# Performance work log

Hardware: AMD Instinct MI355X
Metric: run time of the kernel (lower is better)

## Reference

```python
import jax, jax.numpy as jnp
import numpy as np
import math

N_CELLS = 65536
HIDDEN = 128
IN_DIM = 64
MAX_DEG = 6
BOND_P = 0.5


def _build_graph():
    """2D lattice bond percolation -> padded adjacency [n, MAX_DEG] + signs + mask."""
    rng = np.random.default_rng(0)
    side = int(math.ceil(math.sqrt(N_CELLS)))
    adj = [[] for _ in range(N_CELLS)]
    for i in range(N_CELLS):
        col = i % side
        r = i + 1
        if col + 1 < side and r < N_CELLS and rng.random() < BOND_P:
            adj[i].append(r); adj[r].append(i)
        d = i + side
        if d < N_CELLS and rng.random() < BOND_P:
            adj[i].append(d); adj[d].append(i)
    for i in range(N_CELLS):  # ring fix for isolated nodes
        if not adj[i]:
            r = (i + 1) % N_CELLS
            adj[i].append(r); adj[r].append(i)
    sign_map = {}
    for i in range(N_CELLS):
        for j in adj[i]:
            key = (min(i, j), max(i, j))
            if key not in sign_map:
                sign_map[key] = 1.0 if rng.random() > 0.5 else -1.0
    nbr = np.zeros((N_CELLS, MAX_DEG), np.int32)
    sgn = np.ones((N_CELLS, MAX_DEG), np.float32)
    msk = np.zeros((N_CELLS, MAX_DEG), bool)
    for i in range(N_CELLS):
        for k, j in enumerate(adj[i][:MAX_DEG]):
            nbr[i, k] = j
            msk[i, k] = True
            sgn[i, k] = sign_map[(min(i, j), max(i, j))]
    return nbr, sgn, msk


def setup_inputs() -> dict:
    key = jax.random.key(0)
    ks = jax.random.split(key, 8)
    nbr, sgn, msk = _build_graph()
    n = N_CELLS
    cell_amp = jax.random.uniform(ks[0], (n, HIDDEN)) * 0.5 + 0.5
    cell_phase = jax.random.normal(ks[1], (n, HIDDEN)) * 0.5 \
        + (2.0 * jnp.pi * jnp.arange(n, dtype=jnp.float32) / n)[:, None]
    phase_vel = jax.random.normal(ks[2], (n, HIDDEN)) * 0.05
    return {
        'x': jax.random.normal(ks[3], (1, IN_DIM)),
        'cell_amp': cell_amp.astype(jnp.float32),
        'cell_phase': cell_phase.astype(jnp.float32),
        'phase_vel': phase_vel.astype(jnp.float32),
        'nbr_idx': jnp.asarray(nbr),
        'nbr_sign': jnp.asarray(sgn),
        'nbr_mask': jnp.asarray(msk),
        'W_in': jax.random.normal(ks[4], (HIDDEN, IN_DIM)) * 0.05,
        'b_in': jax.random.normal(ks[5], (HIDDEN,)) * 0.05,
        'W_dec': jax.random.normal(ks[6], (IN_DIM, 2 * HIDDEN)) * 0.05,
        'b_dec': jax.random.normal(ks[7], (IN_DIM,)) * 0.05,
        'step': 1,
    }


def reference(x, cell_amp, cell_phase, phase_vel, nbr_idx, nbr_sign, nbr_mask,
              W_in, b_in, W_dec, b_dec, step):
    n, h = cell_amp.shape
    # complex cell states, then phase-velocity rotation
    states = (cell_amp * jnp.exp(1j * cell_phase)).astype(jnp.complex64)
    states = states * jnp.exp(1j * phase_vel * 0.1)
    ang = jnp.angle(states)                               # [n, h]

    # --- neighbor interference (vectorized gather over padded adjacency) ---
    nbr_states = states[nbr_idx]                          # [n, d, h]
    nbr_ang = ang[nbr_idx]                                # [n, d, h]
    coupling = jnp.cos(ang[:, None, :] - nbr_ang) * nbr_sign[:, :, None]
    contrib = jnp.where(nbr_mask[:, :, None], coupling * nbr_states * 0.1, 0.0)
    interference = contrib.sum(axis=1)                    # [n, h]
    deg = nbr_mask.sum(axis=-1)                           # [n]
    new = 0.7 * states + 0.3 * interference / jnp.maximum(deg, 1)[:, None]
    new = jnp.where((deg > 0)[:, None], new, states)      # 'continue' for isolated nodes

    # --- morphism toward strongest neighbor (argmax over neighbors) ---
    strength = jnp.abs(states).sum(axis=-1)               # [n]
    nstr = jnp.where(nbr_mask, strength[nbr_idx], -jnp.inf)
    best_slot = jnp.argmax(nstr, axis=1)                  # first max, like python max()
    best = jnp.take_along_axis(nbr_idx, best_slot[:, None], axis=1)[:, 0]
    src = states[best]                                    # [n, h]
    morph = jnp.abs(src) * jnp.exp(1j * (jnp.angle(new) - jnp.angle(src)))
    new = jnp.where((deg >= 2)[:, None], new + 0.02 * morph, new)

    # --- global traveling wave ---
    t = step * 0.1
    wave = 0.02 * jnp.sin(t + 2.0 * jnp.pi * jnp.arange(n, dtype=jnp.float32) / n)
    new = new * (1.0 + wave)[:, None]

    # --- input-driven phase perturbation on first 32 cells ---
    sig = x[0] @ W_in.T + b_in                            # [h]
    pp = sig / (jnp.abs(sig).max() + 1e-8) * jnp.pi * 0.1
    idx = jnp.arange(n, dtype=jnp.float32)
    factor = jnp.where(jnp.arange(n) < 32, 0.1 / (1.0 + 0.1 * idx), 0.0)
    new_ang = jnp.angle(new) + pp[None, :] * factor[:, None]
    new = jnp.abs(new) * jnp.exp(1j * new_ang)

    # --- amplitude renormalization per cell ---
    amp = jnp.abs(new)
    amp = amp / (amp.max(axis=-1, keepdims=True) + 1e-8)
    cs = (amp * jnp.exp(1j * jnp.angle(new))).astype(jnp.complex64)

    # --- readout ---
    mean_state = cs.mean(axis=0)                          # [h]
    out_real = jnp.concatenate([mean_state.real, mean_state.imag])[None, :]
    pred = out_real @ W_dec.T + b_dec                     # [1, IN_DIM]
    tension = jnp.var(jnp.abs(cs), ddof=1)                # torch.var (unbiased)
    return pred, tension
```

## Files before the change

kernel.cpp:

```cpp
#include <hip/hip_runtime.h>
#include <hip/hip_fp16.h>
#include <math.h>

#define N_CELLS 65536
#define HIDDEN  128
#define IN_DIM  64
#define MAX_DEG 6

#define WPB    4
#define NPB    32
#define NBLK   (N_CELLS/NPB)
#define CHUNK  4
#define NXCD   8

#define INV2PI 0.15915494309189535f

__device__ __forceinline__ void fsincos(float x, float& s, float& c) {
    const float r = x * INV2PI;
    s = __builtin_amdgcn_sinf(r);
    c = __builtin_amdgcn_cosf(r);
}

#define WS_PP    0
#define WS_FLAG  512
#define WS_STR   1024
#define WS_S     (1024 + N_CELLS*4)
#define WS_P     (WS_S + (size_t)N_CELLS*512)
#define WS_SA    (WS_P + 256*NBLK*4)
#define WS_SA2   (WS_SA + NBLK*4)
#define WS_MEAN  (WS_SA2 + NBLK*4)

__global__ __launch_bounds__(256) void k_pre(
    const float* __restrict__ amp, const float* __restrict__ phase,
    const float* __restrict__ vel,
    const float* __restrict__ x, const float* __restrict__ W_in,
    const float* __restrict__ b_in, const unsigned char* __restrict__ maskb,
    int4* __restrict__ S, float* __restrict__ strength,
    float* __restrict__ pp, int* __restrict__ flag)
{
    const int tid = threadIdx.x;
    if (blockIdx.x < N_CELLS/8) {
        const int node = blockIdx.x*8 + (tid >> 5);
        const int hl   = tid & 31;
        const size_t ro = (size_t)node*HIDDEN + 4*hl;
        const float4 a = *(const float4*)(amp   + ro);
        const float4 p = *(const float4*)(phase + ro);
        const float4 v = *(const float4*)(vel   + ro);
        float s0,c0,s1,c1,s2,c2,s3,c3;
        fsincos(fmaf(0.1f, v.x, p.x), s0, c0);
        fsincos(fmaf(0.1f, v.y, p.y), s1, c1);
        fsincos(fmaf(0.1f, v.z, p.z), s2, c2);
        fsincos(fmaf(0.1f, v.w, p.w), s3, c3);
        union { int4 v4; __half2 h[4]; } u;
        u.h[0] = __floats2half2_rn(a.x*c0, a.x*s0);
        u.h[1] = __floats2half2_rn(a.y*c1, a.y*s1);
        u.h[2] = __floats2half2_rn(a.z*c2, a.z*s2);
        u.h[3] = __floats2half2_rn(a.w*c3, a.w*s3);
        S[(size_t)node*32 + hl] = u.v4;
        float st = a.x + a.y + a.z + a.w;
        #pragma unroll
        for (int off = 16; off > 0; off >>= 1) st += __shfl_xor(st, off);
        if (hl == 0) strength[node] = st;
        return;
    }
    __shared__ float sig[HIDDEN];
    __shared__ float red[HIDDEN];
    __shared__ int fl[256];
    if (tid < HIDDEN) {
        float acc = b_in[tid];
        #pragma unroll 8
        for (int d = 0; d < IN_DIM; ++d) acc = fmaf(W_in[tid*IN_DIM + d], x[d], acc);
        sig[tid] = acc;
        red[tid] = fabsf(acc);
    }
    int v = 0;
    #pragma unroll
    for (int r = 0; r < 4; ++r) v |= (int)maskb[(tid + 256*r)*4 + 1];
    fl[tid] = v;
    __syncthreads();
    for (int s = 64; s > 0; s >>= 1) {
        if (tid < s) red[tid] = fmaxf(red[tid], red[tid + s]);
        __syncthreads();
    }
    for (int s = 128; s > 0; s >>= 1) {
        if (tid < s) fl[tid] |= fl[tid + s];
        __syncthreads();
    }
    if (tid < HIDDEN) pp[tid] = sig[tid] / (red[0] + 1e-8f) * 0.314159265358979f;
    if (tid == 0) *flag = (fl[0] != 0) ? 1 : 0;
}

__global__ __launch_bounds__(256) void k_mainc(
    const int4* __restrict__ S, const int* __restrict__ nbr_idx,
    const float* __restrict__ nbr_sign, const void* __restrict__ nbr_mask,
    const int* __restrict__ step, const float* __restrict__ pp,
    const int* __restrict__ flagp, const float* __restrict__ strength,
    float* __restrict__ P, float* __restrict__ p_sa, float* __restrict__ p_sa2)
{
    __shared__ int   lji[NPB][MAX_DEG];
    __shared__ float lsk[NPB][MAX_DEG];
    __shared__ int   lwp[NPB][8];
    __shared__ int   kmx[NPB/2];
    __shared__ float4 lredre[WPB][32], lredim[WPB][32];
    __shared__ float  lsa[WPB], lsa2[WPB];

    const int tid   = threadIdx.x;
    const int bx    = blockIdx.x;
    const int blk   = (bx & (NXCD-1)) * (NBLK/NXCD) + (bx >> 3);
    const int node0 = blk * NPB;

    if (tid < NPB*MAX_DEG) {
        const int flagv = *flagp;
        const unsigned char* mb = (const unsigned char*)nbr_mask;
        const int*           mi = (const int*)nbr_mask;
        const int n = tid / MAX_DEG, k = tid - n*MAX_DEG;
        const int e = (node0 + n)*MAX_DEG + k;
        const int m = flagv ? (mb[e] != 0) : (mi[e] != 0);
        const int j = nbr_idx[e];
        const float sg = nbr_sign[e];
        lji[n][k] = m ? (j | ((sg < 0.0f) ? (1<<24) : 0) | (1<<25)) : 0;
        lsk[n][k] = m ? strength[j] : -3.0e38f;
    }
    __syncthreads();
    if (tid < NPB) {
        int cnt = 0;
        #pragma unroll
        for (int k = 0; k < MAX_DEG; ++k) {
            const int w = lji[tid][k];
            const float sv = lsk[tid][k];
            if (w >> 25) { lwp[tid][cnt] = w; lsk[tid][cnt] = sv; ++cnt; }
        }
        #pragma unroll
        for (int k = 0; k < MAX_DEG; ++k) if (k >= cnt) lwp[tid][k] = 0;
        int cb = 0; float bv = lsk[tid][0];
        #pragma unroll
        for (int k = 1; k < MAX_DEG; ++k)
            if (k < cnt && lsk[tid][k] > bv) { bv = lsk[tid][k]; cb = k; }
        lwp[tid][6] = cnt;
        lwp[tid][7] = cb;
    }
    __syncthreads();
    if (tid < NPB/2) kmx[tid] = max(lwp[2*tid][6], lwp[2*tid+1][6]);
    __syncthreads();

    const int wv   = tid >> 6;
    const int lane = tid & 63;
    const int half = lane >> 5;
    const int lh   = lane & 31;
    const float trev = 0.1f * (float)step[0] * INV2PI;
    const float4 ppv = ((const float4*)pp)[lh];

    float accre[4] = {0,0,0,0}, accim[4] = {0,0,0,0};
    float accsa = 0.f, accsa2 = 0.f;

    #pragma unroll 1
    for (int c = 0; c < CHUNK; ++c) {
        const int nl = wv*(2*CHUNK) + 2*c + half;
        const int i  = node0 + nl;
        const int4 A0 = *(const int4*)&lwp[nl][0];
        const int4 A1 = *(const int4*)&lwp[nl][4];
        const int deg = A1.z, cb = A1.w;
        const int kmax = kmx[wv*CHUNK + c];

        const int slots[MAX_DEG] = {A0.x, A0.y, A0.z, A0.w, A1.x, A1.y};

        union H { int4 v4; __half2 h[4]; int w[4]; };
        H us, nb[MAX_DEG];
        us.v4 = S[(size_t)(unsigned)i*32 + lh];
        #pragma unroll
        for (int k = 0; k < MAX_DEG; ++k)
            if (k < kmax) nb[k].v4 = S[(size_t)(unsigned)(slots[k] & 0xFFFF)*32 + lh];

        float R[4], I[4], inva[4];
        #pragma unroll
        for (int q = 0; q < 4; ++q) {
            const float2 e = __half22float2(us.h[q]);
            R[q] = e.x; I[q] = e.y;
            inva[q] = __builtin_amdgcn_rsqf(e.x*e.x + e.y*e.y);
        }

        float ir[4] = {0,0,0,0}, ii[4] = {0,0,0,0};
        #pragma unroll
        for (int k = 0; k < MAX_DEG; ++k) {
            if (k < kmax) {
                const int w = slots[k];
                const float sgnm = (w & (1<<25)) ? ((w & (1<<24)) ? -1.0f : 1.0f) : 0.0f;
                #pragma unroll
                for (int q = 0; q < 4; ++q) {
                    const float2 e = __half22float2(nb[k].h[q]);
                    const float E = R[q]*e.x + I[q]*e.y;
                    const float g = sgnm * E * __builtin_amdgcn_rsqf(e.x*e.x + e.y*e.y);
                    ir[q] = fmaf(g, e.x, ir[q]);
                    ii[q] = fmaf(g, e.y, ii[q]);
                }
            }
        }

        H ub;
        #pragma unroll
        for (int q = 0; q < 4; ++q) {
            int v = nb[0].w[q];
            #pragma unroll
            for (int k = 1; k < MAX_DEG; ++k)
                if (k < kmax) v = (k == cb) ? nb[k].w[q] : v;
            ub.w[q] = v;
        }

        const float f = 0.03f * __builtin_amdgcn_rcpf((float)deg);
        float nr[4], ni[4];
        #pragma unroll
        for (int q = 0; q < 4; ++q) {
            const float fq = f * inva[q];
            nr[q] = fmaf(0.7f, R[q], fq*ir[q]);
            ni[q] = fmaf(0.7f, I[q], fq*ii[q]);
        }

        if (deg >= 2) {
            #pragma unroll
            for (int q = 0; q < 4; ++q) {
                const float2 e = __half22float2(ub.h[q]);
                const float im = 0.02f * __builtin_amdgcn_rsqf(nr[q]*nr[q] + ni[q]*ni[q]);
                const float mr = im*(nr[q]*e.x + ni[q]*e.y);
                const float mi = im*(ni[q]*e.x - nr[q]*e.y);
                nr[q] += mr; ni[q] += mi;
            }
        }

        const float wr = fmaf((float)i, 1.52587890625e-5f, trev);
        const float wf = 1.0f + 0.02f * __builtin_amdgcn_sinf(wr);
        #pragma unroll
        for (int q = 0; q < 4; ++q) { nr[q] *= wf; ni[q] *= wf; }

        if (i < 32) {
            const float fac = 0.1f / fmaf(0.1f, (float)i, 1.0f);
            const float pv[4] = {ppv.x, ppv.y, ppv.z, ppv.w};
            #pragma unroll
            for (int q = 0; q < 4; ++q) {
                float sp, cp;
                fsincos(pv[q]*fac, sp, cp);
                const float tr = nr[q]*cp - ni[q]*sp;
                ni[q] = ni[q]*cp + nr[q]*sp;
                nr[q] = tr;
            }
        }

        float m[4];
        #pragma unroll
        for (int q = 0; q < 4; ++q) m[q] = sqrtf(nr[q]*nr[q] + ni[q]*ni[q]);
        float lm = fmaxf(fmaxf(m[0], m[1]), fmaxf(m[2], m[3]));
        #pragma unroll
        for (int off = 16; off > 0; off >>= 1) lm = fmaxf(lm, __shfl_xor(lm, off));
        const float sc = 1.0f / (lm + 1e-8f);
        #pragma unroll
        for (int q = 0; q < 4; ++q) {
            accre[q] += nr[q]*sc;
            accim[q] += ni[q]*sc;
            const float A = m[q]*sc;
            accsa  += A;
            accsa2 += A*A;
        }
    }

    #pragma unroll
    for (int q = 0; q < 4; ++q) {
        accre[q] += __shfl_xor(accre[q], 32);
        accim[q] += __shfl_xor(accim[q], 32);
    }
    #pragma unroll
    for (int off = 32; off > 0; off >>= 1) {
        accsa  += __shfl_xor(accsa,  off);
        accsa2 += __shfl_xor(accsa2, off);
    }
    if (half == 0) {
        lredre[wv][lh] = make_float4(accre[0], accre[1], accre[2], accre[3]);
        lredim[wv][lh] = make_float4(accim[0], accim[1], accim[2], accim[3]);
    }
    if (lane == 0) { lsa[wv] = accsa; lsa2[wv] = accsa2; }
    __syncthreads();
    if (tid < 32) {
        float4 r = lredre[0][tid], im = lredim[0][tid];
        #pragma unroll
        for (int w = 1; w < WPB; ++w) {
            const float4 a = lredre[w][tid], b = lredim[w][tid];
            r.x += a.x; r.y += a.y; r.z += a.z; r.w += a.w;
            im.x += b.x; im.y += b.y; im.z += b.z; im.w += b.w;
        }
        P[(4*tid  )*NBLK + blk]       = r.x;
        P[(4*tid+1)*NBLK + blk]       = r.y;
        P[(4*tid+2)*NBLK + blk]       = r.z;
        P[(4*tid+3)*NBLK + blk]       = r.w;
        P[(128+4*tid  )*NBLK + blk]   = im.x;
        P[(128+4*tid+1)*NBLK + blk]   = im.y;
        P[(128+4*tid+2)*NBLK + blk]   = im.z;
        P[(128+4*tid+3)*NBLK + blk]   = im.w;
    }
    if (tid == 0) {
        p_sa [blk] = lsa[0]  + lsa[1]  + lsa[2]  + lsa[3];
        p_sa2[blk] = lsa2[0] + lsa2[1] + lsa2[2] + lsa2[3];
    }
}

__global__ void k_red(const float* __restrict__ P, float* __restrict__ mean)
{
    __shared__ double red[256];
    const int r = blockIdx.x, tid = threadIdx.x;
    double s = 0.0;
    #pragma unroll
    for (int k = 0; k < NBLK/256; ++k) s += (double)P[(size_t)r*NBLK + tid + 256*k];
    red[tid] = s;
    __syncthreads();
    for (int st = 128; st > 0; st >>= 1) { if (tid < st) red[tid] += red[tid + st]; __syncthreads(); }
    if (tid == 0) mean[r] = (float)(red[0] / (double)N_CELLS);
}

__global__ void k_final(const float* __restrict__ mean_in,
                        const float* __restrict__ p_sa, const float* __restrict__ p_sa2,
                        const float* __restrict__ W_dec, const float* __restrict__ b_dec,
                        float* __restrict__ out)
{
    __shared__ float  mean[2*HIDDEN];
    __shared__ double dred[256];
    __shared__ double tots[2];
    const int tid = threadIdx.x;
    mean[tid] = mean_in[tid];
    double sa = 0.0, sa2 = 0.0;
    #pragma unroll
    for (int k = 0; k < NBLK/256; ++k) {
        sa  += (double)p_sa [tid + 256*k];
        sa2 += (double)p_sa2[tid + 256*k];
    }
    dred[tid] = sa;
    __syncthreads();
    for (int s = 128; s > 0; s >>= 1) { if (tid < s) dred[tid] += dred[tid + s]; __syncthreads(); }
    if (tid == 0) tots[0] = dred[0];
    __syncthreads();
    dred[tid] = sa2;
    __syncthreads();
    for (int s = 128; s > 0; s >>= 1) { if (tid < s) dred[tid] += dred[tid + s]; __syncthreads(); }
    if (tid == 0) tots[1] = dred[0];
    __syncthreads();

    if (tid < IN_DIM) {
        float acc = b_dec[tid];
        #pragma unroll 8
        for (int c = 0; c < 2*HIDDEN; ++c) acc = fmaf(mean[c], W_dec[tid*2*HIDDEN + c], acc);
        out[tid] = acc;
    }
    if (tid == 0) {
        const double M = (double)N_CELLS * (double)HIDDEN;
        const double var = (tots[1] - tots[0]*tots[0]/M) / (M - 1.0);
        out[IN_DIM] = (float)var;
    }
}

extern "C" void kernel_launch(void* const* d_in, const int* in_sizes, int n_in,
                              void* d_out, int out_size, void* d_ws, size_t ws_size,
                              hipStream_t stream)
{
    const float* x       = (const float*)d_in[0];
    const float* amp     = (const float*)d_in[1];
    const float* phase   = (const float*)d_in[2];
    const float* vel     = (const float*)d_in[3];
    const int*   nbr_idx = (const int*)d_in[4];
    const float* nbr_sgn = (const float*)d_in[5];
    const void*  nbr_msk = d_in[6];
    const float* W_in    = (const float*)d_in[7];
    const float* b_in    = (const float*)d_in[8];
    const float* W_dec   = (const float*)d_in[9];
    const float* b_dec   = (const float*)d_in[10];
    const int*   step    = (const int*)d_in[11];

    char* wsb = (char*)d_ws;
    float* pp    = (float*)(wsb + WS_PP);
    int*   flag  = (int*)  (wsb + WS_FLAG);
    float* strg  = (float*)(wsb + WS_STR);
    int4*  S     = (int4*) (wsb + WS_S);
    float* P     = (float*)(wsb + WS_P);
    float* p_sa  = (float*)(wsb + WS_SA);
    float* p_sa2 = (float*)(wsb + WS_SA2);
    float* meanb = (float*)(wsb + WS_MEAN);
    float* out   = (float*)d_out;

    k_pre<<<N_CELLS/8 + 1, 256, 0, stream>>>(amp, phase, vel, x, W_in, b_in,
                                             (const unsigned char*)nbr_msk,
                                             S, strg, pp, flag);
    k_mainc<<<NBLK, 256, 0, stream>>>(S, nbr_idx, nbr_sgn, nbr_msk,
                                      step, pp, flag, strg, P, p_sa, p_sa2);
    k_red<<<256, 256, 0, stream>>>(P, meanb);
    k_final<<<1, 256, 0, stream>>>(meanb, p_sa, p_sa2, W_dec, b_dec, out);
}
```

Baseline: 67.78 us.

## Precompute compacted adjacency in separate kernel and prefetch it in main loop

Measured after the change: 69.57 us. +2.6%, slower.

```diff
diff --git a/kernel.cpp b/kernel.cpp
--- a/kernel.cpp
+++ b/kernel.cpp
@@ -25,7 +25,8 @@
 #define WS_FLAG  512
 #define WS_STR   1024
 #define WS_S     (1024 + N_CELLS*4)
-#define WS_P     (WS_S + (size_t)N_CELLS*512)
+#define WS_ADJ   (WS_S + (size_t)N_CELLS*512)
+#define WS_P     (WS_ADJ + (size_t)N_CELLS*32)
 #define WS_SA    (WS_P + 256*NBLK*4)
 #define WS_SA2   (WS_SA + NBLK*4)
 #define WS_MEAN  (WS_SA2 + NBLK*4)
@@ -90,17 +91,46 @@
     if (tid == 0) *flag = (fl[0] != 0) ? 1 : 0;
 }
 
+__global__ __launch_bounds__(256) void k_adj(
+    const int* __restrict__ nbr_idx, const float* __restrict__ nbr_sign,
+    const void* __restrict__ nbr_mask, const int* __restrict__ flagp,
+    const float* __restrict__ strength, int4* __restrict__ adj)
+{
+    __shared__ int   lw[256][MAX_DEG];
+    __shared__ float ls[256][MAX_DEG];
+    const int t = threadIdx.x;
+    const int i = blockIdx.x*256 + t;
+    const int flagv = *flagp;
+    const unsigned char* mb = (const unsigned char*)nbr_mask;
+    const int*           mi = (const int*)nbr_mask;
+    int cnt = 0;
+    #pragma unroll
+    for (int k = 0; k < MAX_DEG; ++k) {
+        const int e = i*MAX_DEG + k;
+        const int m = flagv ? (mb[e] != 0) : (mi[e] != 0);
+        const int j = nbr_idx[e];
+        const float sg = nbr_sign[e];
+        if (m) {
+            lw[t][cnt] = j | ((sg < 0.0f) ? (1<<24) : 0) | (1<<25);
+            ls[t][cnt] = strength[j];
+            ++cnt;
+        }
+    }
+    #pragma unroll
+    for (int k = 0; k < MAX_DEG; ++k) if (k >= cnt) lw[t][k] = 0;
+    int cb = 0; float bv = ls[t][0];
+    #pragma unroll
+    for (int k = 1; k < MAX_DEG; ++k)
+        if (k < cnt && ls[t][k] > bv) { bv = ls[t][k]; cb = k; }
+    adj[2*(size_t)i    ] = make_int4(lw[t][0], lw[t][1], lw[t][2], lw[t][3]);
+    adj[2*(size_t)i + 1] = make_int4(lw[t][4], lw[t][5], cnt | (cb << 8), 0);
+}
+
 __global__ __launch_bounds__(256) void k_mainc(
-    const int4* __restrict__ S, const int* __restrict__ nbr_idx,
-    const float* __restrict__ nbr_sign, const void* __restrict__ nbr_mask,
+    const int4* __restrict__ S, const int4* __restrict__ adj,
     const int* __restrict__ step, const float* __restrict__ pp,
-    const int* __restrict__ flagp, const float* __restrict__ strength,
     float* __restrict__ P, float* __restrict__ p_sa, float* __restrict__ p_sa2)
 {
-    __shared__ int   lji[NPB][MAX_DEG];
-    __shared__ float lsk[NPB][MAX_DEG];
-    __shared__ int   lwp[NPB][8];
-    __shared__ int   kmx[NPB/2];
     __shared__ float4 lredre[WPB][32], lredim[WPB][32];
     __shared__ float  lsa[WPB], lsa2[WPB];
 
@@ -108,40 +138,6 @@
     const int bx    = blockIdx.x;
     const int blk   = (bx & (NXCD-1)) * (NBLK/NXCD) + (bx >> 3);
     const int node0 = blk * NPB;
-
-    if (tid < NPB*MAX_DEG) {
-        const int flagv = *flagp;
-        const unsigned char* mb = (const unsigned char*)nbr_mask;
-        const int*           mi = (const int*)nbr_mask;
-        const int n = tid / MAX_DEG, k = tid - n*MAX_DEG;
-        const int e = (node0 + n)*MAX_DEG + k;
-        const int m = flagv ? (mb[e] != 0) : (mi[e] != 0);
-        const int j = nbr_idx[e];
-        const float sg = nbr_sign[e];
-        lji[n][k] = m ? (j | ((sg < 0.0f) ? (1<<24) : 0) | (1<<25)) : 0;
-        lsk[n][k] = m ? strength[j] : -3.0e38f;
-    }
-    __syncthreads();
-    if (tid < NPB) {
-        int cnt = 0;
-        #pragma unroll
-        for (int k = 0; k < MAX_DEG; ++k) {
-            const int w = lji[tid][k];
-            const float sv = lsk[tid][k];
-            if (w >> 25) { lwp[tid][cnt] = w; lsk[tid][cnt] = sv; ++cnt; }
-        }
-        #pragma unroll
-        for (int k = 0; k < MAX_DEG; ++k) if (k >= cnt) lwp[tid][k] = 0;
-        int cb = 0; float bv = lsk[tid][0];
-        #pragma unroll
-        for (int k = 1; k < MAX_DEG; ++k)
-            if (k < cnt && lsk[tid][k] > bv) { bv = lsk[tid][k]; cb = k; }
-        lwp[tid][6] = cnt;
-        lwp[tid][7] = cb;
-    }
-    __syncthreads();
-    if (tid < NPB/2) kmx[tid] = max(lwp[2*tid][6], lwp[2*tid+1][6]);
-    __syncthreads();
 
     const int wv   = tid >> 6;
     const int lane = tid & 63;
@@ -153,15 +149,21 @@
     float accre[4] = {0,0,0,0}, accim[4] = {0,0,0,0};
     float accsa = 0.f, accsa2 = 0.f;
 
+    const int nlbase = wv*(2*CHUNK) + half;
+    int4 A0n = adj[2*(size_t)(node0 + nlbase)    ];
+    int4 A1n = adj[2*(size_t)(node0 + nlbase) + 1];
+
     #pragma unroll 1
     for (int c = 0; c < CHUNK; ++c) {
-        const int nl = wv*(2*CHUNK) + 2*c + half;
+        const int nl = nlbase + 2*c;
         const int i  = node0 + nl;
-        const int4 A0 = *(const int4*)&lwp[nl][0];
-        const int4 A1 = *(const int4*)&lwp[nl][4];
-        const int deg = A1.z, cb = A1.w;
-        const int kmax = kmx[wv*CHUNK + c];
-
+        const int4 A0 = A0n, A1 = A1n;
+        if (c + 1 < CHUNK) {
+            A0n = adj[2*(size_t)(i + 2)    ];
+            A1n = adj[2*(size_t)(i + 2) + 1];
+        }
+        const int deg = A1.z & 0xFF;
+        const int cb  = A1.z >> 8;
         const int slots[MAX_DEG] = {A0.x, A0.y, A0.z, A0.w, A1.x, A1.y};
 
         union H { int4 v4; __half2 h[4]; int w[4]; };
@@ -169,7 +171,7 @@
         us.v4 = S[(size_t)(unsigned)i*32 + lh];
         #pragma unroll
         for (int k = 0; k < MAX_DEG; ++k)
-            if (k < kmax) nb[k].v4 = S[(size_t)(unsigned)(slots[k] & 0xFFFF)*32 + lh];
+            if (k < deg) nb[k].v4 = S[(size_t)(unsigned)(slots[k] & 0xFFFF)*32 + lh];
 
         float R[4], I[4], inva[4];
         #pragma unroll
@@ -182,9 +184,9 @@
         float ir[4] = {0,0,0,0}, ii[4] = {0,0,0,0};
         #pragma unroll
         for (int k = 0; k < MAX_DEG; ++k) {
-            if (k < kmax) {
+            if (k < deg) {
                 const int w = slots[k];
-                const float sgnm = (w & (1<<25)) ? ((w & (1<<24)) ? -1.0f : 1.0f) : 0.0f;
+                const float sgnm = (w & (1<<24)) ? -1.0f : 1.0f;
                 #pragma unroll
                 for (int q = 0; q < 4; ++q) {
                     const float2 e = __half22float2(nb[k].h[q]);
@@ -202,7 +204,7 @@
             int v = nb[0].w[q];
             #pragma unroll
             for (int k = 1; k < MAX_DEG; ++k)
-                if (k < kmax) v = (k == cb) ? nb[k].w[q] : v;
+                if (k < deg) v = (k == cb) ? nb[k].w[q] : v;
             ub.w[q] = v;
         }
 
@@ -375,6 +377,7 @@
     int*   flag  = (int*)  (wsb + WS_FLAG);
     float* strg  = (float*)(wsb + WS_STR);
     int4*  S     = (int4*) (wsb + WS_S);
+    int4*  adjv  = (int4*) (wsb + WS_ADJ);
     float* P     = (float*)(wsb + WS_P);
     float* p_sa  = (float*)(wsb + WS_SA);
     float* p_sa2 = (float*)(wsb + WS_SA2);
@@ -384,8 +387,8 @@
     k_pre<<<N_CELLS/8 + 1, 256, 0, stream>>>(amp, phase, vel, x, W_in, b_in,
                                              (const unsigned char*)nbr_msk,
                                              S, strg, pp, flag);
-    k_mainc<<<NBLK, 256, 0, stream>>>(S, nbr_idx, nbr_sgn, nbr_msk,
-                                      step, pp, flag, strg, P, p_sa, p_sa2);
+    k_adj<<<N_CELLS/256, 256, 0, stream>>>(nbr_idx, nbr_sgn, nbr_msk, flag, strg, adjv);
+    k_mainc<<<NBLK, 256, 0, stream>>>(S, adjv, step, pp, P, p_sa, p_sa2);
     k_red<<<256, 256, 0, stream>>>(P, meanb);
     k_final<<<1, 256, 0, stream>>>(meanb, p_sa, p_sa2, W_dec, b_dec, out);
 }
```
